# Kernel tuning notes

Hardware: AMD Instinct MI355X
Metric: run time of the kernel (lower is better)

## Reference

```python
import jax, jax.numpy as jnp
import numpy as np

NX, NF = 8192, 8192
F_SIZE, OUT_SIZE, D_ATT = 512, 256, 128
N_GRAPHS = 16
NEG_INF = -1e9


def setup_inputs() -> dict:
    key = jax.random.key(0)
    ks = jax.random.split(key, 10)
    f = jax.random.normal(ks[0], (NF, F_SIZE), dtype=jnp.float32)
    x = jax.random.normal(ks[1], (NX, OUT_SIZE), dtype=jnp.float32)
    h = jax.random.normal(ks[2], (NX, OUT_SIZE), dtype=jnp.float32)
    edge_index = jax.random.randint(ks[3], (2, NX), 0, NX)
    edge_type = jax.random.randint(ks[4], (NX,), 0, 4)
    f_batch = jnp.sort(jax.random.randint(ks[5], (NF,), 0, N_GRAPHS))
    x_batch = jnp.sort(jax.random.randint(ks[6], (NX,), 0, N_GRAPHS))
    x_init = jax.random.normal(ks[7], (NX, OUT_SIZE), dtype=jnp.float32)
    # Glorot-initialized projection weights, stored [in, out]
    def glorot(k, shape):
        lim = np.sqrt(6.0 / (shape[0] + shape[1]))
        return jax.random.uniform(k, shape, jnp.float32, -lim, lim)
    W_h = glorot(ks[8], (OUT_SIZE, D_ATT))
    kk, kv = jax.random.split(ks[9])
    W_key = glorot(kk, (F_SIZE, D_ATT))
    W_value = glorot(kv, (F_SIZE, OUT_SIZE))
    return {"f": f, "x": x, "h": h, "edge_index": edge_index,
            "edge_type": edge_type, "f_batch": f_batch, "x_batch": x_batch,
            "x_init": x_init, "W_h": W_h, "W_key": W_key, "W_value": W_value}


def reference(f, x, h, edge_index, edge_type, f_batch, x_batch, x_init,
              W_h, W_key, W_value):
    # QKV projections (bias-free linears)
    query = h @ W_h          # [Nx, 128]
    key = f @ W_key          # [Nf, 128]
    value = f @ W_value      # [Nf, out_size]
    # Block-diagonal batch mask: attend only within the same graph
    not_same = x_batch[:, None] != f_batch[None, :]       # [Nx, Nf]
    scores = jnp.einsum('qd,kd->qk', query, key)          # [Nx, Nf]
    scores = jnp.where(not_same, NEG_INF, scores)
    attn = jax.nn.softmax(scores, axis=-1)
    context = attn @ value                                 # [Nx, out_size]
    return context, attn
```

## Files before the change

### kernel.cpp

```cpp
#include <hip/hip_runtime.h>

#define NX_  8192
#define NF_  8192
#define DQ_  128
#define OUT_ 256
#define FS_  512

typedef float  f32x4  __attribute__((ext_vector_type(4)));
typedef short  bf16x8 __attribute__((ext_vector_type(8)));

static __device__ __forceinline__ void nt_store4(const float4& w, float* p) {
  f32x4 v; v.x = w.x; v.y = w.y; v.z = w.z; v.w = w.w;
  __builtin_nontemporal_store(v, (f32x4*)p);
}
static __device__ __forceinline__ ushort f2bf(float f) {
  union { float f; uint u; } c; c.f = f;
  uint r = c.u + 0x7FFF + ((c.u >> 16) & 1);
  return (ushort)(r >> 16);
}
static __device__ __forceinline__ float bf2f(ushort u) {
  union { uint u; float f; } c; c.u = ((uint)u) << 16; return c.f;
}

__global__ void ranges_kernel(const int* __restrict__ xb, const int* __restrict__ fb,
                              int* __restrict__ rng) {
  int t = threadIdx.x;
  if (t < 17) {
    int lo = 0, hi = NX_;
    while (lo < hi) { int mid = (lo + hi) >> 1; if (xb[mid] < t) lo = mid + 1; else hi = mid; }
    rng[t] = lo;
  } else if (t < 34) {
    int g = t - 17;
    int lo = 0, hi = NF_;
    while (lo < hi) { int mid = (lo + hi) >> 1; if (fb[mid] < g) lo = mid + 1; else hi = mid; }
    rng[17 + g] = lo;
  }
}

__global__ __launch_bounds__(256) void zero_attn(float* __restrict__ attn) {
  const size_t n4 = (size_t)NX_ * NF_ / 4;
  size_t stride = (size_t)gridDim.x * 256;
  float4 z = make_float4(0.f, 0.f, 0.f, 0.f);
  for (size_t i = (size_t)blockIdx.x * 256 + threadIdx.x; i < n4; i += stride)
    nt_store4(z, attn + (i << 2));
}

__global__ __launch_bounds__(256) void wprep_kernel(const float* __restrict__ Wh,
                                                    const float* __restrict__ Wk,
                                                    const float* __restrict__ Wv,
                                                    ushort* __restrict__ WhTh, ushort* __restrict__ WhTl,
                                                    ushort* __restrict__ WkTh, ushort* __restrict__ WkTl,
                                                    ushort* __restrict__ WvTh, ushort* __restrict__ WvTl) {
  int idx = blockIdx.x * 256 + threadIdx.x;
  float w; ushort* ph; ushort* pl; int off;
  if (idx < 32768) {
    int n = idx >> 8, k = idx & 255;
    w = Wh[k * DQ_ + n]; ph = WhTh; pl = WhTl; off = idx;
  } else if (idx < 98304) {
    int i = idx - 32768; int n = i >> 9, k = i & 511;
    w = Wk[k * DQ_ + n]; ph = WkTh; pl = WkTl; off = i;
  } else if (idx < 229376) {
    int i = idx - 98304; int n = i >> 9, k = i & 511;
    w = Wv[k * OUT_ + n]; ph = WvTh; pl = WvTl; off = i;
  } else return;
  ushort hi = f2bf(w);
  ph[off] = hi;
  pl[off] = f2bf(w - bf2f(hi));
}

__global__ __launch_bounds__(256) void prep_split(const float* __restrict__ f,
                                                  const float* __restrict__ h,
                                                  ushort* __restrict__ fh, ushort* __restrict__ fl,
                                                  ushort* __restrict__ hh, ushort* __restrict__ hl) {
  const int NF4 = (NF_ * FS_) / 4;
  const int NH4 = (NX_ * OUT_) / 4;
  int stride = gridDim.x * 256;
  for (int i = blockIdx.x * 256 + threadIdx.x; i < NF4 + NH4; i += stride) {
    const float4* src; ushort* ph; ushort* pl; int j;
    if (i < NF4) { src = (const float4*)f; ph = fh; pl = fl; j = i; }
    else         { src = (const float4*)h; ph = hh; pl = hl; j = i - NF4; }
    float4 v = src[j];
    ushort4 uh, ul;
    uh.x = f2bf(v.x); ul.x = f2bf(v.x - bf2f(uh.x));
    uh.y = f2bf(v.y); ul.y = f2bf(v.y - bf2f(uh.y));
    uh.z = f2bf(v.z); ul.z = f2bf(v.z - bf2f(uh.z));
    uh.w = f2bf(v.w); ul.w = f2bf(v.w - bf2f(uh.w));
    ((ushort4*)ph)[j] = uh;
    ((ushort4*)pl)[j] = ul;
  }
}

__global__ __launch_bounds__(256) void gemm_all(const ushort* __restrict__ fh, const ushort* __restrict__ fl,
                                                const ushort* __restrict__ hh, const ushort* __restrict__ hl,
                                                const ushort* __restrict__ WhTh, const ushort* __restrict__ WhTl,
                                                const ushort* __restrict__ WkTh, const ushort* __restrict__ WkTl,
                                                const ushort* __restrict__ WvTh,
                                                ushort* __restrict__ Qh, ushort* __restrict__ Ql,
                                                ushort* __restrict__ Kh, ushort* __restrict__ Kl,
                                                ushort* __restrict__ VT) {
  __shared__ ushort Ahi[64][64], Alo[64][64];
  __shared__ ushort Bhi[64][64], Blo[64][64];
  int bid = blockIdx.x;
  const ushort *Ah, *Al, *BTh, *BTl;
  int N, K, lid, mode;
  if (bid < 256)      { Ah = hh; Al = hl; BTh = WhTh; BTl = WhTl; N = DQ_;  K = OUT_; mode = 0; lid = bid; }
  else if (bid < 512) { Ah = fh; Al = fl; BTh = WkTh; BTl = WkTl; N = DQ_;  K = FS_;  mode = 1; lid = bid - 256; }
  else                { Ah = fh; Al = fh; BTh = WvTh; BTl = WvTh; N = OUT_; K = FS_;  mode = 2; lid = bid - 512; }
  int nbn = N >> 6;
  int bm = (lid / nbn) << 6, bn = (lid % nbn) << 6;
  int tid = threadIdx.x, lane = tid & 63, w = tid >> 6;
  int srow = tid >> 2, skq = (tid & 3) << 4;
  bool split = (mode < 2);
  f32x4 acc[4];
#pragma unroll
  for (int i = 0; i < 4; ++i) acc[i] = (f32x4){0.f, 0.f, 0.f, 0.f};

  for (int k0 = 0; k0 < K; k0 += 64) {
    size_t aoff = (size_t)(bm + srow) * K + k0 + skq;
    size_t boff = (size_t)(bn + srow) * K + k0 + skq;
#pragma unroll
    for (int j = 0; j < 2; ++j) {
      int sk = (skq + (j << 3)) ^ ((srow & 7) << 3);
      *(uint4*)&Ahi[srow][sk] = *(const uint4*)(Ah + aoff + (j << 3));
      *(uint4*)&Bhi[srow][sk] = *(const uint4*)(BTh + boff + (j << 3));
      if (split) {
        *(uint4*)&Alo[srow][sk] = *(const uint4*)(Al + aoff + (j << 3));
        *(uint4*)&Blo[srow][sk] = *(const uint4*)(BTl + boff + (j << 3));
      }
    }
    __syncthreads();
#pragma unroll
    for (int step = 0; step < 2; ++step) {
      int kb = (step << 5) + ((lane >> 4) << 3);
      int brow = (w << 4) + (lane & 15);
      int bsk = kb ^ ((brow & 7) << 3);
      bf16x8 bh = *(const bf16x8*)&Bhi[brow][bsk];
#pragma unroll
      for (int i = 0; i < 4; ++i) {
        int ar = (i << 4) + (lane & 15);
        int ask = kb ^ ((ar & 7) << 3);
        bf16x8 ah = *(const bf16x8*)&Ahi[ar][ask];
        acc[i] = __builtin_amdgcn_mfma_f32_16x16x32_bf16(ah, bh, acc[i], 0, 0, 0);
        if (split) {
          bf16x8 bl = *(const bf16x8*)&Blo[brow][bsk];
          bf16x8 al = *(const bf16x8*)&Alo[ar][ask];
          acc[i] = __builtin_amdgcn_mfma_f32_16x16x32_bf16(al, bh, acc[i], 0, 0, 0);
          acc[i] = __builtin_amdgcn_mfma_f32_16x16x32_bf16(ah, bl, acc[i], 0, 0, 0);
        }
      }
    }
    __syncthreads();
  }
  int cr = (lane >> 4) << 2, cc = lane & 15;
  if (mode < 2) {
    ushort* Ch = (mode == 0) ? Qh : Kh;
    ushort* Cl = (mode == 0) ? Ql : Kl;
#pragma unroll
    for (int i = 0; i < 4; ++i)
#pragma unroll
      for (int r = 0; r < 4; ++r) {
        float v = acc[i][r];
        ushort hi = f2bf(v);
        size_t o = (size_t)(bm + (i << 4) + cr + r) * DQ_ + bn + (w << 4) + cc;
        Ch[o] = hi;
        Cl[o] = f2bf(v - bf2f(hi));
      }
  } else {
#pragma unroll
    for (int i = 0; i < 4; ++i) {
      ushort4 o;
      o.x = f2bf(acc[i][0]); o.y = f2bf(acc[i][1]);
      o.z = f2bf(acc[i][2]); o.w = f2bf(acc[i][3]);
      *(ushort4*)&VT[(size_t)(bn + (w << 4) + cc) * NX_ + bm + (i << 4) + cr] = o;
    }
  }
}

__global__ __launch_bounds__(256) void fused_attn(const ushort* __restrict__ Qh, const ushort* __restrict__ Ql,
                                                  const ushort* __restrict__ Kh, const ushort* __restrict__ Kl,
                                                  const ushort* __restrict__ VT,
                                                  const int* __restrict__ xb,
                                                  const int* __restrict__ rng,
                                                  float* __restrict__ attn,
                                                  float* __restrict__ ctx) {
  __shared__ ushort Pb[16][784];
  __shared__ float wred[8][16];
  int r0 = blockIdx.x << 4;
  int tid = threadIdx.x;
  int w = tid >> 6, lane = tid & 63;
  int lg = lane >> 4, li = lane & 15;
  int g0 = xb[r0], g1 = xb[r0 + 15];
  for (int g = g0; g <= g1; ++g) {
    int rs = rng[g], re = rng[g + 1];
    int ars = (rs > r0 ? rs : r0) - r0;
    int are = (re < r0 + 16 ? re : r0 + 16) - r0;
    if (ars >= are) continue;
    int ks = rng[17 + g], ke = rng[18 + g];
    int kbase = ks & ~7;
    const ushort* qrh = Qh + (size_t)(r0 + li) * DQ_ + (lg << 3);
    const ushort* qrl = Ql + (size_t)(r0 + li) * DQ_ + (lg << 3);
    bf16x8 qh[4], ql[4];
#pragma unroll
    for (int db = 0; db < 4; ++db) {
      qh[db] = *(const bf16x8*)(qrh + (db << 5));
      ql[db] = *(const bf16x8*)(qrl + (db << 5));
    }
    f32x4 s[12];
#pragma unroll
    for (int tt = 0; tt < 12; ++tt) {
      int key0 = kbase + (((tt << 2) + w) << 4);
      int krow = key0 + li; if (krow > NF_ - 1) krow = NF_ - 1;
      const ushort* krh = Kh + (size_t)krow * DQ_ + (lg << 3);
      const ushort* krl = Kl + (size_t)krow * DQ_ + (lg << 3);
      f32x4 a = (f32x4){0.f, 0.f, 0.f, 0.f};
#pragma unroll
      for (int db = 0; db < 4; ++db) {
        bf16x8 kh = *(const bf16x8*)(krh + (db << 5));
        bf16x8 kl = *(const bf16x8*)(krl + (db << 5));
        a = __builtin_amdgcn_mfma_f32_16x16x32_bf16(qh[db], kh, a, 0, 0, 0);
        a = __builtin_amdgcn_mfma_f32_16x16x32_bf16(ql[db], kh, a, 0, 0, 0);
        a = __builtin_amdgcn_mfma_f32_16x16x32_bf16(qh[db], kl, a, 0, 0, 0);
      }
      s[tt] = a;
    }
    float pm[4];
#pragma unroll
    for (int r = 0; r < 4; ++r) pm[r] = -3.0e38f;
#pragma unroll
    for (int tt = 0; tt < 12; ++tt) {
      int col = kbase + (((tt << 2) + w) << 4) + li;
      bool valid = (col >= ks) && (col < ke);
#pragma unroll
      for (int r = 0; r < 4; ++r) pm[r] = fmaxf(pm[r], valid ? s[tt][r] : -3.0e38f);
    }
#pragma unroll
    for (int r = 0; r < 4; ++r) {
      pm[r] = fmaxf(pm[r], __shfl_xor(pm[r], 1));
      pm[r] = fmaxf(pm[r], __shfl_xor(pm[r], 2));
      pm[r] = fmaxf(pm[r], __shfl_xor(pm[r], 4));
      pm[r] = fmaxf(pm[r], __shfl_xor(pm[r], 8));
    }
    if (li == 0) {
#pragma unroll
      for (int r = 0; r < 4; ++r) wred[w][(lg << 2) + r] = pm[r];
    }
    __syncthreads();
    float m[4], ps[4];
#pragma unroll
    for (int r = 0; r < 4; ++r) {
      int row = (lg << 2) + r;
      m[r] = fmaxf(fmaxf(wred[0][row], wred[1][row]), fmaxf(wred[2][row], wred[3][row]));
      ps[r] = 0.f;
    }
#pragma unroll
    for (int tt = 0; tt < 12; ++tt) {
      int col = kbase + (((tt << 2) + w) << 4) + li;
      bool valid = (col >= ks) && (col < ke);
#pragma unroll
      for (int r = 0; r < 4; ++r) {
        float e = valid ? __expf(s[tt][r] - m[r]) : 0.f;
        s[tt][r] = e;
        ps[r] += e;
      }
    }
#pragma unroll
    for (int r = 0; r < 4; ++r) {
      ps[r] += __shfl_xor(ps[r], 1);
      ps[r] += __shfl_xor(ps[r], 2);
      ps[r] += __shfl_xor(ps[r], 4);
      ps[r] += __shfl_xor(ps[r], 8);
    }
    if (li == 0) {
#pragma unroll
      for (int r = 0; r < 4; ++r) wred[4 + w][(lg << 2) + r] = ps[r];
    }
    __syncthreads();
    float inv[4];
#pragma unroll
    for (int r = 0; r < 4; ++r) {
      int row = (lg << 2) + r;
      inv[r] = 1.0f / (wred[4][row] + wred[5][row] + wred[6][row] + wred[7][row]);
    }
#pragma unroll
    for (int tt = 0; tt < 12; ++tt) {
      int kc = (((tt << 2) + w) << 4) + li;
#pragma unroll
      for (int r = 0; r < 4; ++r)
        Pb[(lg << 2) + r][kc] = f2bf(s[tt][r] * inv[r]);
    }
    __syncthreads();
    for (int idx = tid; idx < 16 * 192; idx += 256) {
      int row = idx / 192;
      if (row < ars || row >= are) continue;
      int c4 = idx - row * 192;
      int col = kbase + (c4 << 2);
      if (col >= NF_) continue;
      ushort4 pu = *(const ushort4*)&Pb[row][c4 << 2];
      float4 wv;
      wv.x = bf2f(pu.x); wv.y = bf2f(pu.y); wv.z = bf2f(pu.z); wv.w = bf2f(pu.w);
      nt_store4(wv, attn + (size_t)(r0 + row) * NF_ + col);
    }
    int nsteps = (ke - kbase + 31) >> 5;
    f32x4 pacc[4];
#pragma unroll
    for (int ot = 0; ot < 4; ++ot) pacc[ot] = (f32x4){0.f, 0.f, 0.f, 0.f};
    for (int st = 0; st < nsteps; ++st) {
      bf16x8 pfr = *(const bf16x8*)&Pb[li][(st << 5) + (lg << 3)];
      int kaddr = kbase + (st << 5) + (lg << 3);
      if (kaddr > NF_ - 8) kaddr = NF_ - 8;
#pragma unroll
      for (int ot = 0; ot < 4; ++ot) {
        const ushort* vr = VT + (size_t)((w << 6) + (ot << 4) + li) * NX_ + kaddr;
        bf16x8 vfr = *(const bf16x8*)vr;
        pacc[ot] = __builtin_amdgcn_mfma_f32_16x16x32_bf16(pfr, vfr, pacc[ot], 0, 0, 0);
      }
    }
#pragma unroll
    for (int ot = 0; ot < 4; ++ot)
#pragma unroll
      for (int r = 0; r < 4; ++r) {
        int row = (lg << 2) + r;
        if (row >= ars && row < are)
          ctx[(size_t)(r0 + row) * OUT_ + (w << 6) + (ot << 4) + li] = pacc[ot][r];
      }
    __syncthreads();
  }
}

extern "C" void kernel_launch(void* const* d_in, const int* in_sizes, int n_in,
                              void* d_out, int out_size, void* d_ws, size_t ws_size,
                              hipStream_t stream) {
  const float* f   = (const float*)d_in[0];
  const float* h   = (const float*)d_in[2];
  const int*   fb  = (const int*)d_in[5];
  const int*   xbt = (const int*)d_in[6];
  const float* Wh  = (const float*)d_in[8];
  const float* Wk  = (const float*)d_in[9];
  const float* Wv  = (const float*)d_in[10];

  float* ctx_out  = (float*)d_out;
  float* attn_out = ctx_out + (size_t)NX_ * OUT_;

  ushort* fh   = (ushort*)d_ws;
  ushort* fl   = fh + (size_t)NF_ * FS_;
  ushort* hh   = fl + (size_t)NF_ * FS_;
  ushort* hl   = hh + (size_t)NX_ * OUT_;
  ushort* Qh   = hl + (size_t)NX_ * OUT_;
  ushort* Ql   = Qh + (size_t)NX_ * DQ_;
  ushort* Kh   = Ql + (size_t)NX_ * DQ_;
  ushort* Kl   = Kh + (size_t)NF_ * DQ_;
  ushort* VT   = Kl + (size_t)NF_ * DQ_;
  ushort* WhTh = VT + (size_t)OUT_ * NX_;
  ushort* WhTl = WhTh + 32768;
  ushort* WkTh = WhTl + 32768;
  ushort* WkTl = WkTh + 65536;
  ushort* WvTh = WkTl + 65536;
  ushort* WvTl = WvTh + 131072;
  int*    rng  = (int*)(WvTl + 131072);

  hipLaunchKernelGGL(ranges_kernel, dim3(1), dim3(64), 0, stream, xbt, fb, rng);
  hipLaunchKernelGGL(zero_attn, dim3(4096), dim3(256), 0, stream, attn_out);
  hipLaunchKernelGGL(wprep_kernel, dim3(896), dim3(256), 0, stream,
                     Wh, Wk, Wv, WhTh, WhTl, WkTh, WkTl, WvTh, WvTl);
  hipLaunchKernelGGL(prep_split, dim3(2048), dim3(256), 0, stream,
                     f, h, fh, fl, hh, hl);
  hipLaunchKernelGGL(gemm_all, dim3(1024), dim3(256), 0, stream,
                     fh, fl, hh, hl, WhTh, WhTl, WkTh, WkTl, WvTh,
                     Qh, Ql, Kh, Kl, VT);
  hipLaunchKernelGGL(fused_attn, dim3(NX_ / 16), dim3(256), 0, stream,
                     Qh, Ql, Kh, Kl, VT, xbt, rng, attn_out, ctx_out);
}
```

Measured before the change: 445.0 us.

## Fuse attn zero-fill into attention kernel and widen blocks to 512 threads

Drops the separate pass that zero-filled the whole attention matrix. The fused attention kernel now writes each full output row itself: softmax values inside the group's key window and zeros everywhere else, so each element of the large output is written once instead of twice. The attention kernel also moves to 8 waves per block, so each wave owns half as many key tiles and output columns. It remaps block IDs with a swizzle across XCD-like groups and hoists the Q fragment loads out of the per-group loop. The cost is more per-block store work and a different register/occupancy profile.

```diff
diff --git a/kernel.cpp b/kernel.cpp
--- a/kernel.cpp
+++ b/kernel.cpp
@@ -35,14 +35,6 @@
     while (lo < hi) { int mid = (lo + hi) >> 1; if (fb[mid] < g) lo = mid + 1; else hi = mid; }
     rng[17 + g] = lo;
   }
-}
-
-__global__ __launch_bounds__(256) void zero_attn(float* __restrict__ attn) {
-  const size_t n4 = (size_t)NX_ * NF_ / 4;
-  size_t stride = (size_t)gridDim.x * 256;
-  float4 z = make_float4(0.f, 0.f, 0.f, 0.f);
-  for (size_t i = (size_t)blockIdx.x * 256 + threadIdx.x; i < n4; i += stride)
-    nt_store4(z, attn + (i << 2));
 }
 
 __global__ __launch_bounds__(256) void wprep_kernel(const float* __restrict__ Wh,
@@ -176,7 +168,7 @@
   }
 }
 
-__global__ __launch_bounds__(256) void fused_attn(const ushort* __restrict__ Qh, const ushort* __restrict__ Ql,
+__global__ __launch_bounds__(512) void fused_attn(const ushort* __restrict__ Qh, const ushort* __restrict__ Ql,
                                                   const ushort* __restrict__ Kh, const ushort* __restrict__ Kl,
                                                   const ushort* __restrict__ VT,
                                                   const int* __restrict__ xb,
@@ -184,11 +176,21 @@
                                                   float* __restrict__ attn,
                                                   float* __restrict__ ctx) {
   __shared__ ushort Pb[16][784];
-  __shared__ float wred[8][16];
-  int r0 = blockIdx.x << 4;
+  __shared__ float wred[16][16];
+  int bid = blockIdx.x;
+  int sb = ((bid & 7) << 6) | (bid >> 3);
+  int r0 = sb << 4;
   int tid = threadIdx.x;
   int w = tid >> 6, lane = tid & 63;
   int lg = lane >> 4, li = lane & 15;
+  const ushort* qrh = Qh + (size_t)(r0 + li) * DQ_ + (lg << 3);
+  const ushort* qrl = Ql + (size_t)(r0 + li) * DQ_ + (lg << 3);
+  bf16x8 qh[4], ql[4];
+#pragma unroll
+  for (int db = 0; db < 4; ++db) {
+    qh[db] = *(const bf16x8*)(qrh + (db << 5));
+    ql[db] = *(const bf16x8*)(qrl + (db << 5));
+  }
   int g0 = xb[r0], g1 = xb[r0 + 15];
   for (int g = g0; g <= g1; ++g) {
     int rs = rng[g], re = rng[g + 1];
@@ -197,18 +199,10 @@
     if (ars >= are) continue;
     int ks = rng[17 + g], ke = rng[18 + g];
     int kbase = ks & ~7;
-    const ushort* qrh = Qh + (size_t)(r0 + li) * DQ_ + (lg << 3);
-    const ushort* qrl = Ql + (size_t)(r0 + li) * DQ_ + (lg << 3);
-    bf16x8 qh[4], ql[4];
-#pragma unroll
-    for (int db = 0; db < 4; ++db) {
-      qh[db] = *(const bf16x8*)(qrh + (db << 5));
-      ql[db] = *(const bf16x8*)(qrl + (db << 5));
-    }
-    f32x4 s[12];
-#pragma unroll
-    for (int tt = 0; tt < 12; ++tt) {
-      int key0 = kbase + (((tt << 2) + w) << 4);
+    f32x4 s[6];
+#pragma unroll
+    for (int tt = 0; tt < 6; ++tt) {
+      int key0 = kbase + (((tt << 3) + w) << 4);
       int krow = key0 + li; if (krow > NF_ - 1) krow = NF_ - 1;
       const ushort* krh = Kh + (size_t)krow * DQ_ + (lg << 3);
       const ushort* krl = Kl + (size_t)krow * DQ_ + (lg << 3);
@@ -227,8 +221,8 @@
 #pragma unroll
     for (int r = 0; r < 4; ++r) pm[r] = -3.0e38f;
 #pragma unroll
-    for (int tt = 0; tt < 12; ++tt) {
-      int col = kbase + (((tt << 2) + w) << 4) + li;
+    for (int tt = 0; tt < 6; ++tt) {
+      int col = kbase + (((tt << 3) + w) << 4) + li;
       bool valid = (col >= ks) && (col < ke);
 #pragma unroll
       for (int r = 0; r < 4; ++r) pm[r] = fmaxf(pm[r], valid ? s[tt][r] : -3.0e38f);
@@ -249,12 +243,16 @@
 #pragma unroll
     for (int r = 0; r < 4; ++r) {
       int row = (lg << 2) + r;
-      m[r] = fmaxf(fmaxf(wred[0][row], wred[1][row]), fmaxf(wred[2][row], wred[3][row]));
+      float m01 = fmaxf(wred[0][row], wred[1][row]);
+      float m23 = fmaxf(wred[2][row], wred[3][row]);
+      float m45 = fmaxf(wred[4][row], wred[5][row]);
+      float m67 = fmaxf(wred[6][row], wred[7][row]);
+      m[r] = fmaxf(fmaxf(m01, m23), fmaxf(m45, m67));
       ps[r] = 0.f;
     }
 #pragma unroll
-    for (int tt = 0; tt < 12; ++tt) {
-      int col = kbase + (((tt << 2) + w) << 4) + li;
+    for (int tt = 0; tt < 6; ++tt) {
+      int col = kbase + (((tt << 3) + w) << 4) + li;
       bool valid = (col >= ks) && (col < ke);
 #pragma unroll
       for (int r = 0; r < 4; ++r) {
@@ -272,56 +270,59 @@
     }
     if (li == 0) {
 #pragma unroll
-      for (int r = 0; r < 4; ++r) wred[4 + w][(lg << 2) + r] = ps[r];
+      for (int r = 0; r < 4; ++r) wred[8 + w][(lg << 2) + r] = ps[r];
     }
     __syncthreads();
     float inv[4];
 #pragma unroll
     for (int r = 0; r < 4; ++r) {
       int row = (lg << 2) + r;
-      inv[r] = 1.0f / (wred[4][row] + wred[5][row] + wred[6][row] + wred[7][row]);
-    }
-#pragma unroll
-    for (int tt = 0; tt < 12; ++tt) {
-      int kc = (((tt << 2) + w) << 4) + li;
+      float s0 = wred[8][row] + wred[9][row] + wred[10][row] + wred[11][row];
+      float s1 = wred[12][row] + wred[13][row] + wred[14][row] + wred[15][row];
+      inv[r] = 1.0f / (s0 + s1);
+    }
+#pragma unroll
+    for (int tt = 0; tt < 6; ++tt) {
+      int kc = (((tt << 3) + w) << 4) + li;
 #pragma unroll
       for (int r = 0; r < 4; ++r)
         Pb[(lg << 2) + r][kc] = f2bf(s[tt][r] * inv[r]);
     }
     __syncthreads();
-    for (int idx = tid; idx < 16 * 192; idx += 256) {
-      int row = idx / 192;
+    for (int idx = tid; idx < 16 * (NF_ / 4); idx += 512) {
+      int row = idx >> 11;
       if (row < ars || row >= are) continue;
-      int c4 = idx - row * 192;
-      int col = kbase + (c4 << 2);
-      if (col >= NF_) continue;
-      ushort4 pu = *(const ushort4*)&Pb[row][c4 << 2];
-      float4 wv;
-      wv.x = bf2f(pu.x); wv.y = bf2f(pu.y); wv.z = bf2f(pu.z); wv.w = bf2f(pu.w);
+      int col = (idx & 2047) << 2;
+      float4 wv = make_float4(0.f, 0.f, 0.f, 0.f);
+      int rel = col - kbase;
+      if (rel >= 0 && rel < 768) {
+        ushort4 pu = *(const ushort4*)&Pb[row][rel];
+        wv.x = bf2f(pu.x); wv.y = bf2f(pu.y); wv.z = bf2f(pu.z); wv.w = bf2f(pu.w);
+      }
       nt_store4(wv, attn + (size_t)(r0 + row) * NF_ + col);
     }
     int nsteps = (ke - kbase + 31) >> 5;
-    f32x4 pacc[4];
-#pragma unroll
-    for (int ot = 0; ot < 4; ++ot) pacc[ot] = (f32x4){0.f, 0.f, 0.f, 0.f};
+    f32x4 pacc[2];
+#pragma unroll
+    for (int ot = 0; ot < 2; ++ot) pacc[ot] = (f32x4){0.f, 0.f, 0.f, 0.f};
     for (int st = 0; st < nsteps; ++st) {
       bf16x8 pfr = *(const bf16x8*)&Pb[li][(st << 5) + (lg << 3)];
       int kaddr = kbase + (st << 5) + (lg << 3);
       if (kaddr > NF_ - 8) kaddr = NF_ - 8;
 #pragma unroll
-      for (int ot = 0; ot < 4; ++ot) {
-        const ushort* vr = VT + (size_t)((w << 6) + (ot << 4) + li) * NX_ + kaddr;
+      for (int ot = 0; ot < 2; ++ot) {
+        const ushort* vr = VT + (size_t)((w << 5) + (ot << 4) + li) * NX_ + kaddr;
         bf16x8 vfr = *(const bf16x8*)vr;
         pacc[ot] = __builtin_amdgcn_mfma_f32_16x16x32_bf16(pfr, vfr, pacc[ot], 0, 0, 0);
       }
     }
 #pragma unroll
-    for (int ot = 0; ot < 4; ++ot)
+    for (int ot = 0; ot < 2; ++ot)
 #pragma unroll
       for (int r = 0; r < 4; ++r) {
         int row = (lg << 2) + r;
         if (row >= ars && row < are)
-          ctx[(size_t)(r0 + row) * OUT_ + (w << 6) + (ot << 4) + li] = pacc[ot][r];
+          ctx[(size_t)(r0 + row) * OUT_ + (w << 5) + (ot << 4) + li] = pacc[ot][r];
       }
     __syncthreads();
   }
@@ -359,7 +360,6 @@
   int*    rng  = (int*)(WvTl + 131072);
 
   hipLaunchKernelGGL(ranges_kernel, dim3(1), dim3(64), 0, stream, xbt, fb, rng);
-  hipLaunchKernelGGL(zero_attn, dim3(4096), dim3(256), 0, stream, attn_out);
   hipLaunchKernelGGL(wprep_kernel, dim3(896), dim3(256), 0, stream,
                      Wh, Wk, Wv, WhTh, WhTl, WkTh, WkTl, WvTh, WvTl);
   hipLaunchKernelGGL(prep_split, dim3(2048), dim3(256), 0, stream,
@@ -367,6 +367,6 @@
   hipLaunchKernelGGL(gemm_all, dim3(1024), dim3(256), 0, stream,
                      fh, fl, hh, hl, WhTh, WhTl, WkTh, WkTl, WvTh,
                      Qh, Ql, Kh, Kl, VT);
-  hipLaunchKernelGGL(fused_attn, dim3(NX_ / 16), dim3(256), 0, stream,
+  hipLaunchKernelGGL(fused_attn, dim3(NX_ / 16), dim3(512), 0, stream,
                      Qh, Ql, Kh, Kl, VT, xbt, rng, attn_out, ctx_out);
 }
```

Result: faster. 425.7 us (-4.3%).
